# Performance work log

Measured on AMD Instinct MI355X. Metric: run time of the kernel, lower is better.

The kernel has to match this reference:

```python
import jax, jax.numpy as jnp
import numpy as np

N_NODES = 50000
N_EDGES = 800000
D = 256


def setup_inputs() -> dict:
    key = jax.random.key(0)
    k_x, k_e, k_w1, k_w2 = jax.random.split(key, 4)
    x = jax.random.normal(k_x, (N_NODES, D), dtype=jnp.float32)
    edge_index = jax.random.randint(k_e, (2, N_EDGES), 0, N_NODES, dtype=jnp.int64)
    # attention MLP params (Linear(d, d//2) -> ReLU -> Linear(d//2, 1) -> Sigmoid)
    W1 = jax.random.normal(k_w1, (D, D // 2), dtype=jnp.float32) * (1.0 / np.sqrt(D))
    b1 = jnp.zeros((D // 2,), dtype=jnp.float32)
    W2 = jax.random.normal(k_w2, (D // 2, 1), dtype=jnp.float32) * (1.0 / np.sqrt(D // 2))
    b2 = jnp.zeros((1,), dtype=jnp.float32)
    return {"x": x, "edge_index": edge_index, "W1": W1, "b1": b1, "W2": W2, "b2": b2}


def reference(x, edge_index, W1, b1, W2, b2):
    # mean aggregation with attention: for each destination node i (row),
    # weighted mean of neighbor (col) features with sigmoid-MLP attention weights.
    row, col = edge_index[0], edge_index[1]
    neigh = x[col]                                   # [E, D] gathered neighbor features
    h = jax.nn.relu(neigh @ W1 + b1)                 # [E, D//2]
    w = jax.nn.sigmoid(h @ W2 + b2)                  # [E, 1] attention weight per edge
    num = jax.ops.segment_sum(neigh * w, row, num_segments=N_NODES)  # [N, D]
    den = jax.ops.segment_sum(w, row, num_segments=N_NODES)          # [N, 1]
    # nodes with no neighbors stay zero (matching the torch loop's skip)
    out = jnp.where(den > 0, num / jnp.maximum(den, 1e-12), 0.0)
    return out
```

## Files before the change

### kernel.cpp

```cpp
#include <hip/hip_runtime.h>
#include <hip/hip_bf16.h>

#define D 256
#define DH 128
#define NB 8

typedef __attribute__((ext_vector_type(8))) short short8;
typedef __attribute__((ext_vector_type(4))) float floatx4;

__global__ __launch_bounds__(256) void detect_kernel(const int* __restrict__ ei,
                                                     int* __restrict__ flag, int E) {
    int tid = threadIdx.x;
    int limit = min(E, 4096);
    int v = 0;
    for (int i = tid; i < limit; i += 256) v |= ei[2 * i + 1];
#pragma unroll
    for (int off = 32; off > 0; off >>= 1) v |= __shfl_down(v, off, 64);
    if ((tid & 63) == 0) atomicOr(flag, v);
}

__device__ __forceinline__ int eload(const void* p, long long i, int is64) {
    if (is64) return (int)((const long long*)p)[i];
    return ((const int*)p)[i];
}

__device__ __forceinline__ unsigned pack_bf16(unsigned a, unsigned b) {
    unsigned ra = (a + 0x7fffu + ((a >> 16) & 1u)) >> 16;
    unsigned rb = (b + 0x7fffu + ((b >> 16) & 1u)) & 0xffff0000u;
    return ra | rb;
}
__device__ __forceinline__ unsigned short bf16_of(float f) {
    unsigned u = __float_as_uint(f);
    return (unsigned short)((u + 0x7fffu + ((u >> 16) & 1u)) >> 16);
}

__global__ __launch_bounds__(256) void pack_w1_kernel(const float* __restrict__ W1,
                                                      uint4* __restrict__ Bp) {
    int t = blockIdx.x * 256 + threadIdx.x;
    int lane = t & 63;
    int kt = (t >> 6) & 7;
    int nt = t >> 9;
    int col = nt * 16 + (lane & 15);
    int k0 = kt * 32 + (lane >> 4) * 8;
    unsigned v[8];
#pragma unroll
    for (int j = 0; j < 8; ++j) v[j] = __float_as_uint(W1[(k0 + j) * DH + col]);
    uint4 o;
    o.x = pack_bf16(v[0], v[1]);
    o.y = pack_bf16(v[2], v[3]);
    o.z = pack_bf16(v[4], v[5]);
    o.w = pack_bf16(v[6], v[7]);
    Bp[t] = o;
}

__global__ __launch_bounds__(256) void score_scatter_kernel(
        const float* __restrict__ x, const uint4* __restrict__ Bp,
        const float* __restrict__ b1, const float* __restrict__ W2,
        const float* __restrict__ b2, uint2* __restrict__ xb,
        float* __restrict__ s,
        const void* __restrict__ ep, const int* __restrict__ flag,
        int* __restrict__ cursor, unsigned short* __restrict__ cols,
        int cap, int N, int E, int TB) {
    if ((int)blockIdx.x < TB) {
        int is64 = (*flag == 0);
        int e = blockIdx.x * 256 + threadIdx.x;
        if (e < E) {
            int r = eload(ep, e, is64);
            int c = eload(ep, (long long)E + e, is64);
            int p = atomicAdd(&cursor[r], 1);
            if (p < cap) cols[(size_t)r * cap + p] = (unsigned short)c;
        }
        return;
    }
    int blk = blockIdx.x - TB;
    int tid = threadIdx.x;
    long long n64 = (long long)N * 64;

    long long gbase = (long long)blk * 4096 + tid;
#pragma unroll 4
    for (int i = 0; i < 16; ++i) {
        long long g = gbase + i * 256;
        if (g < n64) {
            uint4 f = ((const uint4*)x)[g];
            uint2 o;
            o.x = pack_bf16(f.x, f.y);
            o.y = pack_bf16(f.z, f.w);
            xb[g] = o;
        }
    }

    int lane = tid & 63;
    int wid = tid >> 6;
    int quad = lane >> 4;
    int rbase = blk * 64 + wid * 16;

    int arow = rbase + (lane & 15);
    bool rv = arow < N;
    const float* xr = x + (size_t)(rv ? arow : 0) * D + quad * 8;

    short8 afrag[8];
#pragma unroll
    for (int kt = 0; kt < 8; ++kt) {
        float4 f0 = make_float4(0.f, 0.f, 0.f, 0.f), f1 = f0;
        if (rv) {
            f0 = ((const float4*)(xr + kt * 32))[0];
            f1 = ((const float4*)(xr + kt * 32))[1];
        }
        short8 a;
        a.s0 = (short)bf16_of(f0.x); a.s1 = (short)bf16_of(f0.y);
        a.s2 = (short)bf16_of(f0.z); a.s3 = (short)bf16_of(f0.w);
        a.s4 = (short)bf16_of(f1.x); a.s5 = (short)bf16_of(f1.y);
        a.s6 = (short)bf16_of(f1.z); a.s7 = (short)bf16_of(f1.w);
        afrag[kt] = a;
    }

    float z0 = 0.f, z1 = 0.f, z2 = 0.f, z3 = 0.f;
#pragma unroll
    for (int nt = 0; nt < 8; ++nt) {
        floatx4 acc = {0.f, 0.f, 0.f, 0.f};
#pragma unroll
        for (int kt = 0; kt < 8; ++kt) {
            uint4 braw = Bp[(nt * 8 + kt) * 64 + lane];
            short8 b;
            b.s0 = (short)(braw.x & 0xffff); b.s1 = (short)(braw.x >> 16);
            b.s2 = (short)(braw.y & 0xffff); b.s3 = (short)(braw.y >> 16);
            b.s4 = (short)(braw.z & 0xffff); b.s5 = (short)(braw.z >> 16);
            b.s6 = (short)(braw.w & 0xffff); b.s7 = (short)(braw.w >> 16);
            acc = __builtin_amdgcn_mfma_f32_16x16x32_bf16(afrag[kt], b, acc, 0, 0, 0);
        }
        int col = nt * 16 + (lane & 15);
        float b1c = b1[col], w2c = W2[col];
        z0 += fmaxf(acc[0] + b1c, 0.f) * w2c;
        z1 += fmaxf(acc[1] + b1c, 0.f) * w2c;
        z2 += fmaxf(acc[2] + b1c, 0.f) * w2c;
        z3 += fmaxf(acc[3] + b1c, 0.f) * w2c;
    }

#pragma unroll
    for (int off = 1; off < 16; off <<= 1) {
        z0 += __shfl_xor(z0, off, 64);
        z1 += __shfl_xor(z1, off, 64);
        z2 += __shfl_xor(z2, off, 64);
        z3 += __shfl_xor(z3, off, 64);
    }
    if ((lane & 15) == 0) {
        float b2v = b2[0];
        int r = rbase + quad * 4;
        float zz[4] = {z0, z1, z2, z3};
#pragma unroll
        for (int j = 0; j < 4; ++j)
            if (r + j < N) s[r + j] = 1.f / (1.f + __expf(-(zz[j] + b2v)));
    }
}

__device__ __forceinline__ float4 unpack_bf16x4(uint2 v) {
    float4 r;
    r.x = __uint_as_float(v.x << 16);
    r.y = __uint_as_float(v.x & 0xffff0000u);
    r.z = __uint_as_float(v.y << 16);
    r.w = __uint_as_float(v.y & 0xffff0000u);
    return r;
}

__global__ __launch_bounds__(256) void agg_u16_kernel(const uint2* __restrict__ xb,
                                                      const float* __restrict__ s,
                                                      const int* __restrict__ cursor,
                                                      const unsigned short* __restrict__ cols,
                                                      int cap,
                                                      float4* __restrict__ out4, int N) {
    int lane = threadIdx.x & 63;
    int node = blockIdx.x * 4 + (threadIdx.x >> 6);
    if (node >= N) return;
    int cnt = min(cursor[node], cap);
    const unsigned short* mc = cols + (size_t)node * cap;

    float4 acc = make_float4(0.f, 0.f, 0.f, 0.f);
    float den = 0.f;
    int k = 0;
    for (; k + 4 <= cnt; k += 4) {
        int c0 = mc[k], c1 = mc[k + 1], c2 = mc[k + 2], c3 = mc[k + 3];
        float s0 = s[c0], s1 = s[c1], s2 = s[c2], s3 = s[c3];
        uint2 v0 = xb[(size_t)c0 * 64 + lane];
        uint2 v1 = xb[(size_t)c1 * 64 + lane];
        uint2 v2 = xb[(size_t)c2 * 64 + lane];
        uint2 v3 = xb[(size_t)c3 * 64 + lane];
        float4 f0 = unpack_bf16x4(v0);
        float4 f1 = unpack_bf16x4(v1);
        float4 f2 = unpack_bf16x4(v2);
        float4 f3 = unpack_bf16x4(v3);
        acc.x = fmaf(f0.x, s0, fmaf(f1.x, s1, fmaf(f2.x, s2, fmaf(f3.x, s3, acc.x))));
        acc.y = fmaf(f0.y, s0, fmaf(f1.y, s1, fmaf(f2.y, s2, fmaf(f3.y, s3, acc.y))));
        acc.z = fmaf(f0.z, s0, fmaf(f1.z, s1, fmaf(f2.z, s2, fmaf(f3.z, s3, acc.z))));
        acc.w = fmaf(f0.w, s0, fmaf(f1.w, s1, fmaf(f2.w, s2, fmaf(f3.w, s3, acc.w))));
        den += (s0 + s1) + (s2 + s3);
    }
    for (; k < cnt; ++k) {
        int c0 = mc[k];
        float s0 = s[c0];
        float4 f0 = unpack_bf16x4(xb[(size_t)c0 * 64 + lane]);
        acc.x = fmaf(f0.x, s0, acc.x);
        acc.y = fmaf(f0.y, s0, acc.y);
        acc.z = fmaf(f0.z, s0, acc.z);
        acc.w = fmaf(f0.w, s0, acc.w);
        den += s0;
    }
    float4 o = make_float4(0.f, 0.f, 0.f, 0.f);
    if (cnt > 0) {
        float inv = 1.f / den;
        o.x = acc.x * inv; o.y = acc.y * inv; o.z = acc.z * inv; o.w = acc.w * inv;
    }
    out4[(size_t)node * 64 + lane] = o;
}

__global__ __launch_bounds__(256) void score_kernel(const float* __restrict__ x,
                                                    const float* __restrict__ W1,
                                                    const float* __restrict__ b1,
                                                    const float* __restrict__ W2,
                                                    const float* __restrict__ b2,
                                                    float* __restrict__ s, int N) {
    __shared__ __align__(16) float xs[4][NB][D];
    int lane = threadIdx.x & 63;
    int wid  = threadIdx.x >> 6;
    int base = (blockIdx.x * 4 + wid) * NB;
#pragma unroll
    for (int m = 0; m < NB; ++m) {
        int n = base + m;
        float4 v = make_float4(0.f, 0.f, 0.f, 0.f);
        if (n < N) v = ((const float4*)x)[(size_t)n * 64 + lane];
        ((float4*)&xs[wid][m][0])[lane] = v;
    }
    __syncthreads();
    float h0[NB], h1[NB];
#pragma unroll
    for (int m = 0; m < NB; ++m) { h0[m] = 0.f; h1[m] = 0.f; }
#pragma unroll 4
    for (int k = 0; k < D; ++k) {
        float w1a = W1[k * DH + lane];
        float w1b = W1[k * DH + 64 + lane];
#pragma unroll
        for (int m = 0; m < NB; ++m) {
            float xv = xs[wid][m][k];
            h0[m] = fmaf(xv, w1a, h0[m]);
            h1[m] = fmaf(xv, w1b, h1[m]);
        }
    }
    float b1a = b1[lane], b1b = b1[lane + 64];
    float w2a = W2[lane], w2b = W2[lane + 64];
    float b2v = b2[0];
#pragma unroll
    for (int m = 0; m < NB; ++m) {
        float za = fmaxf(h0[m] + b1a, 0.f) * w2a + fmaxf(h1[m] + b1b, 0.f) * w2b;
#pragma unroll
        for (int off = 32; off > 0; off >>= 1) za += __shfl_down(za, off, 64);
        if (lane == 0) {
            int n = base + m;
            if (n < N) s[n] = 1.f / (1.f + __expf(-(za + b2v)));
        }
    }
}

__global__ __launch_bounds__(256) void hist_kernel(const void* __restrict__ ep,
                                                   const int* __restrict__ flag,
                                                   int* __restrict__ cnt, int E) {
    int is64 = (*flag == 0);
    int e = blockIdx.x * blockDim.x + threadIdx.x;
    if (e < E) atomicAdd(&cnt[eload(ep, e, is64)], 1);
}

__global__ __launch_bounds__(256) void bucket_kernel(const int* __restrict__ cnt,
                                                     int* __restrict__ beg,
                                                     int* __restrict__ cursor,
                                                     int* __restrict__ total, int N) {
    int i = blockIdx.x * blockDim.x + threadIdx.x;
    int lane = threadIdx.x & 63;
    int v = (i < N) ? cnt[i] : 0;
    int inc = v;
#pragma unroll
    for (int off = 1; off < 64; off <<= 1) {
        int t = __shfl_up(inc, off, 64);
        if (lane >= off) inc += t;
    }
    int base = 0;
    if (lane == 63) base = atomicAdd(total, inc);
    base = __shfl(base, 63, 64);
    if (i < N) {
        int b = base + inc - v;
        beg[i] = b;
        cursor[i] = b;
    }
}

__global__ __launch_bounds__(256) void scatter32_kernel(const void* __restrict__ ep,
                                                        const int* __restrict__ flag,
                                                        int* __restrict__ cursor,
                                                        int* __restrict__ cols, int E) {
    int is64 = (*flag == 0);
    int e = blockIdx.x * blockDim.x + threadIdx.x;
    if (e < E) {
        int r = eload(ep, e, is64);
        int c = eload(ep, (long long)E + e, is64);
        int p = atomicAdd(&cursor[r], 1);
        cols[p] = c;
    }
}

__global__ __launch_bounds__(256) void agg_f32_kernel(const float4* __restrict__ x4,
                                                      const float* __restrict__ s,
                                                      const int* __restrict__ begs,
                                                      const int* __restrict__ cnt,
                                                      const int* __restrict__ cols,
                                                      float4* __restrict__ out4, int N) {
    int lane = threadIdx.x & 63;
    int node = blockIdx.x * 4 + (threadIdx.x >> 6);
    if (node >= N) return;
    int beg = begs[node], end = beg + cnt[node];
    float4 acc = make_float4(0.f, 0.f, 0.f, 0.f);
    float den = 0.f;
    for (int k = beg; k < end; ++k) {
        int c = cols[k];
        float sc = s[c];
        float4 xv = x4[(size_t)c * 64 + lane];
        acc.x = fmaf(xv.x, sc, acc.x);
        acc.y = fmaf(xv.y, sc, acc.y);
        acc.z = fmaf(xv.z, sc, acc.z);
        acc.w = fmaf(xv.w, sc, acc.w);
        den += sc;
    }
    float4 o = make_float4(0.f, 0.f, 0.f, 0.f);
    if (end > beg) {
        float inv = 1.f / den;
        o.x = acc.x * inv; o.y = acc.y * inv; o.z = acc.z * inv; o.w = acc.w * inv;
    }
    out4[(size_t)node * 64 + lane] = o;
}

extern "C" void kernel_launch(void* const* d_in, const int* in_sizes, int n_in,
                              void* d_out, int out_size, void* d_ws, size_t ws_size,
                              hipStream_t stream) {
    const float* x  = (const float*)d_in[0];
    const void*  ei = d_in[1];
    const float* W1 = (const float*)d_in[2];
    const float* b1 = (const float*)d_in[3];
    const float* W2 = (const float*)d_in[4];
    const float* b2 = (const float*)d_in[5];
    int N = in_sizes[0] / D;
    int E = in_sizes[1] / 2;

    char* ws = (char*)d_ws;

    auto plan = [&](int cap, size_t& oCur, size_t& oS, size_t& oCols,
                    size_t& oBp, size_t& oXb) -> size_t {
        oCur  = 16;
        oS    = (oCur + (size_t)N * 4 + 15) & ~15ull;
        oCols = (oS + (size_t)N * 4 + 255) & ~255ull;
        oBp   = (oCols + (size_t)N * cap * 2 + 255) & ~255ull;
        oXb   = (oBp + 65536 + 255) & ~255ull;
        return oXb + (size_t)N * D * 2;
    };

    int cap = 96;
    size_t oCur, oS, oCols, oBp, oXb;
    size_t need = plan(cap, oCur, oS, oCols, oBp, oXb);
    if (need > ws_size) { cap = 64; need = plan(cap, oCur, oS, oCols, oBp, oXb); }

    if (N <= 65536 && need <= ws_size) {
        int*            flag   = (int*)(ws);
        int*            cursor = (int*)(ws + oCur);
        float*          s      = (float*)(ws + oS);
        unsigned short* cols   = (unsigned short*)(ws + oCols);
        uint4*          Bpack  = (uint4*)(ws + oBp);
        uint2*          xb     = (uint2*)(ws + oXb);

        hipMemsetAsync(ws, 0, oCur + (size_t)N * 4, stream);

        detect_kernel<<<1, 256, 0, stream>>>((const int*)ei, flag, E);
        pack_w1_kernel<<<16, 256, 0, stream>>>(W1, Bpack);

        int TB = (E + 255) / 256;
        int SB = (N + 63) / 64;
        score_scatter_kernel<<<TB + SB, 256, 0, stream>>>(x, Bpack, b1, W2, b2,
                                                          xb, s, ei, flag, cursor,
                                                          cols, cap, N, E, TB);
        agg_u16_kernel<<<(N + 3) / 4, 256, 0, stream>>>(xb, s, cursor, cols, cap,
                                                        (float4*)d_out, N);
        return;
    }

    size_t o0 = 0;
    size_t o1 = 16;
    size_t o2 = (o1 + (size_t)N * 4 + 15) & ~15ull;
    size_t o3 = (o2 + (size_t)N * 4 + 15) & ~15ull;
    size_t o4 = (o3 + (size_t)N * 4 + 15) & ~15ull;
    size_t o5 = (o4 + (size_t)N * 4 + 15) & ~15ull;
    int*   flag   = (int*)(ws + o0);
    int*   total  = (int*)(ws + o0 + 4);
    int*   cnt    = (int*)(ws + o1);
    int*   beg    = (int*)(ws + o2);
    int*   cursor = (int*)(ws + o3);
    float* s      = (float*)(ws + o4);
    int*   cols   = (int*)(ws + o5);

    hipMemsetAsync(ws, 0, o1 + (size_t)N * 4, stream);
    detect_kernel<<<1, 256, 0, stream>>>((const int*)ei, flag, E);
    score_kernel<<<(N + 4 * NB - 1) / (4 * NB), 256, 0, stream>>>(x, W1, b1, W2, b2, s, N);
    hist_kernel<<<(E + 255) / 256, 256, 0, stream>>>(ei, flag, cnt, E);
    bucket_kernel<<<(N + 255) / 256, 256, 0, stream>>>(cnt, beg, cursor, total, N);
    scatter32_kernel<<<(E + 255) / 256, 256, 0, stream>>>(ei, flag, cursor, cols, E);
    agg_f32_kernel<<<(N + 3) / 4, 256, 0, stream>>>((const float4*)x, s, beg, cnt, cols,
                                                    (float4*)d_out, N);
}
```

Before: 243.4 us.

## Fuse prep kernels, pad atomic counters, reuse bf16 x tile via LDS

Merges the index-width detect kernel and the W1 packing kernel into one launch. Each scatter thread now handles four edges, and the per-node cursor counters are padded so atomics on different nodes fall on different cache lines. Score blocks now run before the scatter blocks, and the MFMA A fragments are read from an LDS copy of the bf16 tile the block just converted, so x is no longer read and converted twice. The padded counters enlarge the memset and the workspace, and the 64x65 uint2 LDS tile plus a barrier may lower occupancy of the score blocks.

```diff
diff --git a/kernel.cpp b/kernel.cpp
--- a/kernel.cpp
+++ b/kernel.cpp
@@ -7,17 +7,6 @@
 
 typedef __attribute__((ext_vector_type(8))) short short8;
 typedef __attribute__((ext_vector_type(4))) float floatx4;
-
-__global__ __launch_bounds__(256) void detect_kernel(const int* __restrict__ ei,
-                                                     int* __restrict__ flag, int E) {
-    int tid = threadIdx.x;
-    int limit = min(E, 4096);
-    int v = 0;
-    for (int i = tid; i < limit; i += 256) v |= ei[2 * i + 1];
-#pragma unroll
-    for (int off = 32; off > 0; off >>= 1) v |= __shfl_down(v, off, 64);
-    if ((tid & 63) == 0) atomicOr(flag, v);
-}
 
 __device__ __forceinline__ int eload(const void* p, long long i, int is64) {
     if (is64) return (int)((const long long*)p)[i];
@@ -34,8 +23,20 @@
     return (unsigned short)((u + 0x7fffu + ((u >> 16) & 1u)) >> 16);
 }
 
-__global__ __launch_bounds__(256) void pack_w1_kernel(const float* __restrict__ W1,
-                                                      uint4* __restrict__ Bp) {
+__global__ __launch_bounds__(256) void prep_kernel(const float* __restrict__ W1,
+                                                   uint4* __restrict__ Bp,
+                                                   const int* __restrict__ ei,
+                                                   int* __restrict__ flag, int E) {
+    if (blockIdx.x == 16) {
+        int tid = threadIdx.x;
+        int limit = min(E, 4096);
+        int v = 0;
+        for (int i = tid; i < limit; i += 256) v |= ei[2 * i + 1];
+#pragma unroll
+        for (int off = 32; off > 0; off >>= 1) v |= __shfl_down(v, off, 64);
+        if ((tid & 63) == 0) atomicOr(flag, v);
+        return;
+    }
     int t = blockIdx.x * 256 + threadIdx.x;
     int lane = t & 63;
     int kt = (t >> 6) & 7;
@@ -60,59 +61,62 @@
         float* __restrict__ s,
         const void* __restrict__ ep, const int* __restrict__ flag,
         int* __restrict__ cursor, unsigned short* __restrict__ cols,
-        int cap, int N, int E, int TB) {
-    if ((int)blockIdx.x < TB) {
+        int cap, int pad, int N, int E, int SB) {
+    if ((int)blockIdx.x >= SB) {
         int is64 = (*flag == 0);
-        int e = blockIdx.x * 256 + threadIdx.x;
-        if (e < E) {
-            int r = eload(ep, e, is64);
-            int c = eload(ep, (long long)E + e, is64);
-            int p = atomicAdd(&cursor[r], 1);
-            if (p < cap) cols[(size_t)r * cap + p] = (unsigned short)c;
+        int base = (blockIdx.x - SB) * 1024 + threadIdx.x;
+        int r[4], c[4];
+        bool vld[4];
+#pragma unroll
+        for (int j = 0; j < 4; ++j) {
+            int e = base + j * 256;
+            vld[j] = (e < E);
+            if (vld[j]) {
+                r[j] = eload(ep, e, is64);
+                c[j] = eload(ep, (long long)E + e, is64);
+            }
+        }
+#pragma unroll
+        for (int j = 0; j < 4; ++j) {
+            if (vld[j]) {
+                int p = atomicAdd(&cursor[r[j] * pad], 1);
+                if (p < cap) cols[(size_t)r[j] * cap + p] = (unsigned short)c[j];
+            }
         }
         return;
     }
-    int blk = blockIdx.x - TB;
+
+    __shared__ __align__(16) uint2 lds[64 * 65];
     int tid = threadIdx.x;
+    int blk = blockIdx.x;
     long long n64 = (long long)N * 64;
 
     long long gbase = (long long)blk * 4096 + tid;
-#pragma unroll 4
+#pragma unroll
     for (int i = 0; i < 16; ++i) {
         long long g = gbase + i * 256;
+        int idx = i * 256 + tid;
         if (g < n64) {
             uint4 f = ((const uint4*)x)[g];
             uint2 o;
             o.x = pack_bf16(f.x, f.y);
             o.y = pack_bf16(f.z, f.w);
             xb[g] = o;
-        }
-    }
+            lds[(idx >> 6) * 65 + (idx & 63)] = o;
+        }
+    }
+    __syncthreads();
 
     int lane = tid & 63;
     int wid = tid >> 6;
     int quad = lane >> 4;
     int rbase = blk * 64 + wid * 16;
-
-    int arow = rbase + (lane & 15);
-    bool rv = arow < N;
-    const float* xr = x + (size_t)(rv ? arow : 0) * D + quad * 8;
+    int lrow = wid * 16 + (lane & 15);
 
     short8 afrag[8];
 #pragma unroll
-    for (int kt = 0; kt < 8; ++kt) {
-        float4 f0 = make_float4(0.f, 0.f, 0.f, 0.f), f1 = f0;
-        if (rv) {
-            f0 = ((const float4*)(xr + kt * 32))[0];
-            f1 = ((const float4*)(xr + kt * 32))[1];
-        }
-        short8 a;
-        a.s0 = (short)bf16_of(f0.x); a.s1 = (short)bf16_of(f0.y);
-        a.s2 = (short)bf16_of(f0.z); a.s3 = (short)bf16_of(f0.w);
-        a.s4 = (short)bf16_of(f1.x); a.s5 = (short)bf16_of(f1.y);
-        a.s6 = (short)bf16_of(f1.z); a.s7 = (short)bf16_of(f1.w);
-        afrag[kt] = a;
-    }
+    for (int kt = 0; kt < 8; ++kt)
+        afrag[kt] = *(const short8*)&lds[lrow * 65 + kt * 8 + quad * 2];
 
     float z0 = 0.f, z1 = 0.f, z2 = 0.f, z3 = 0.f;
 #pragma unroll
@@ -166,12 +170,12 @@
                                                       const float* __restrict__ s,
                                                       const int* __restrict__ cursor,
                                                       const unsigned short* __restrict__ cols,
-                                                      int cap,
+                                                      int cap, int pad,
                                                       float4* __restrict__ out4, int N) {
     int lane = threadIdx.x & 63;
     int node = blockIdx.x * 4 + (threadIdx.x >> 6);
     if (node >= N) return;
-    int cnt = min(cursor[node], cap);
+    int cnt = min(cursor[node * pad], cap);
     const unsigned short* mc = cols + (size_t)node * cap;
 
     float4 acc = make_float4(0.f, 0.f, 0.f, 0.f);
@@ -210,6 +214,17 @@
         o.x = acc.x * inv; o.y = acc.y * inv; o.z = acc.z * inv; o.w = acc.w * inv;
     }
     out4[(size_t)node * 64 + lane] = o;
+}
+
+__global__ __launch_bounds__(256) void detect_kernel(const int* __restrict__ ei,
+                                                     int* __restrict__ flag, int E) {
+    int tid = threadIdx.x;
+    int limit = min(E, 4096);
+    int v = 0;
+    for (int i = tid; i < limit; i += 256) v |= ei[2 * i + 1];
+#pragma unroll
+    for (int off = 32; off > 0; off >>= 1) v |= __shfl_down(v, off, 64);
+    if ((tid & 63) == 0) atomicOr(flag, v);
 }
 
 __global__ __launch_bounds__(256) void score_kernel(const float* __restrict__ x,
@@ -348,20 +363,22 @@
 
     char* ws = (char*)d_ws;
 
-    auto plan = [&](int cap, size_t& oCur, size_t& oS, size_t& oCols,
+    auto plan = [&](int cap, int pad, size_t& oCur, size_t& oS, size_t& oCols,
                     size_t& oBp, size_t& oXb) -> size_t {
         oCur  = 16;
-        oS    = (oCur + (size_t)N * 4 + 15) & ~15ull;
+        oS    = (oCur + (size_t)N * pad * 4 + 15) & ~15ull;
         oCols = (oS + (size_t)N * 4 + 255) & ~255ull;
         oBp   = (oCols + (size_t)N * cap * 2 + 255) & ~255ull;
         oXb   = (oBp + 65536 + 255) & ~255ull;
         return oXb + (size_t)N * D * 2;
     };
 
-    int cap = 96;
+    int cap = 96, pad = 16;
     size_t oCur, oS, oCols, oBp, oXb;
-    size_t need = plan(cap, oCur, oS, oCols, oBp, oXb);
-    if (need > ws_size) { cap = 64; need = plan(cap, oCur, oS, oCols, oBp, oXb); }
+    size_t need = plan(cap, pad, oCur, oS, oCols, oBp, oXb);
+    if (need > ws_size) { pad = 4;  need = plan(cap, pad, oCur, oS, oCols, oBp, oXb); }
+    if (need > ws_size) { pad = 1;  need = plan(cap, pad, oCur, oS, oCols, oBp, oXb); }
+    if (need > ws_size) { cap = 64; need = plan(cap, pad, oCur, oS, oCols, oBp, oXb); }
 
     if (N <= 65536 && need <= ws_size) {
         int*            flag   = (int*)(ws);
@@ -371,17 +388,16 @@
         uint4*          Bpack  = (uint4*)(ws + oBp);
         uint2*          xb     = (uint2*)(ws + oXb);
 
-        hipMemsetAsync(ws, 0, oCur + (size_t)N * 4, stream);
-
-        detect_kernel<<<1, 256, 0, stream>>>((const int*)ei, flag, E);
-        pack_w1_kernel<<<16, 256, 0, stream>>>(W1, Bpack);
-
-        int TB = (E + 255) / 256;
+        hipMemsetAsync(ws, 0, oCur + (size_t)N * pad * 4, stream);
+
+        prep_kernel<<<17, 256, 0, stream>>>(W1, Bpack, (const int*)ei, flag, E);
+
         int SB = (N + 63) / 64;
-        score_scatter_kernel<<<TB + SB, 256, 0, stream>>>(x, Bpack, b1, W2, b2,
-                                                          xb, s, ei, flag, cursor,
-                                                          cols, cap, N, E, TB);
-        agg_u16_kernel<<<(N + 3) / 4, 256, 0, stream>>>(xb, s, cursor, cols, cap,
+        int TBe = (E + 1023) / 1024;
+        score_scatter_kernel<<<SB + TBe, 256, 0, stream>>>(x, Bpack, b1, W2, b2,
+                                                           xb, s, ei, flag, cursor,
+                                                           cols, cap, pad, N, E, SB);
+        agg_u16_kernel<<<(N + 3) / 4, 256, 0, stream>>>(xb, s, cursor, cols, cap, pad,
                                                         (float4*)d_out, N);
         return;
     }
```

Measured after the change: 214.2 us. 12.0% less time.
